# Kernel optimization log

Hardware: AMD Instinct MI355X
Metric: run time of the kernel (lower is better)

## Reference

```python
import jax, jax.numpy as jnp
import numpy as np

B, S = 2, 1024
V, D, H, L, F, M = 50257, 768, 12, 6, 3072, 1024
DK = D // H
EPS = 1e-5


def _layer_norm(x, g, b):
    mu = jnp.mean(x, axis=-1, keepdims=True)
    var = jnp.mean(jnp.square(x - mu), axis=-1, keepdims=True)
    return (x - mu) * jax.lax.rsqrt(var + EPS) * g + b


def setup_inputs() -> dict:
    key = jax.random.key(0)
    ks = jax.random.split(key, 20)
    std = 0.02
    inp = {
        'input_ids': jax.random.randint(ks[0], (B, S), 0, V),
        'tok_emb': jax.random.normal(ks[1], (V, D), jnp.float32) * std,
        'pos_emb': jax.random.normal(ks[2], (M, D), jnp.float32) * std,
        # per-layer stacked params; linear weights stored as [in, out] (y = x @ W)
        'wq': jax.random.normal(ks[3], (L, D, D), jnp.float32) * std,
        'wk': jax.random.normal(ks[4], (L, D, D), jnp.float32) * std,
        'wv': jax.random.normal(ks[5], (L, D, D), jnp.float32) * std,
        'wo': jax.random.normal(ks[6], (L, D, D), jnp.float32) * std,
        'bo': jnp.zeros((L, D), jnp.float32),
        'fc_w': jax.random.normal(ks[7], (L, D, F), jnp.float32) * std,
        'fc_b': jnp.zeros((L, F), jnp.float32),
        'proj_w': jax.random.normal(ks[8], (L, F, D), jnp.float32) * std,
        'proj_b': jnp.zeros((L, D), jnp.float32),
        'ln1_g': jnp.ones((L, D), jnp.float32),
        'ln1_b': jnp.zeros((L, D), jnp.float32),
        'ln2_g': jnp.ones((L, D), jnp.float32),
        'ln2_b': jnp.zeros((L, D), jnp.float32),
        'lnf_g': jnp.ones((D,), jnp.float32),
        'lnf_b': jnp.zeros((D,), jnp.float32),
        'out_w': jax.random.normal(ks[9], (D, V), jnp.float32) * std,
    }
    return inp


def reference(input_ids, tok_emb, pos_emb, wq, wk, wv, wo, bo, fc_w, fc_b,
              proj_w, proj_b, ln1_g, ln1_b, ln2_g, ln2_b, lnf_g, lnf_b, out_w):
    b, s = input_ids.shape
    x = tok_emb[input_ids] + pos_emb[jnp.arange(s)][None, :, :]  # [B,S,D]
    causal = jnp.tril(jnp.ones((s, s), bool))  # [S,S]
    scale = 1.0 / np.sqrt(DK)
    for l in range(L):
        xn = _layer_norm(x, ln1_g[l], ln1_b[l])
        q = (xn @ wq[l]).reshape(b, s, H, DK).transpose(0, 2, 1, 3)
        k = (xn @ wk[l]).reshape(b, s, H, DK).transpose(0, 2, 1, 3)
        v = (xn @ wv[l]).reshape(b, s, H, DK).transpose(0, 2, 1, 3)
        scores = jnp.einsum('bhqd,bhkd->bhqk', q, k) * scale
        scores = jnp.where(causal[None, None], scores, -1e9)
        attn = jax.nn.softmax(scores, axis=-1)
        ctx = jnp.einsum('bhqk,bhkd->bhqd', attn, v)
        ctx = ctx.transpose(0, 2, 1, 3).reshape(b, s, D)
        x = x + ctx @ wo[l] + bo[l]
        xn = _layer_norm(x, ln2_g[l], ln2_b[l])
        h = jax.nn.gelu(xn @ fc_w[l] + fc_b[l], approximate=False)
        x = x + h @ proj_w[l] + proj_b[l]
    x = _layer_norm(x, lnf_g, lnf_b)
    logits = x @ out_w  # [B,S,V]
    return logits
```

## Files before the change

kernel.cpp:

```cpp
#include <hip/hip_runtime.h>
#include <hip/hip_bf16.h>
#include <math.h>

#define BB 2
#define SS 1024
#define DD 768
#define HH 12
#define LL 6
#define FF 3072
#define VV 50257
#define DKK 64
#define NROWS (BB * SS)
#define QKVN (3 * DD)
#define QBLK 64
#define KVBLK 64

#define OFF_QKV 0
#define OFF_WO  1769472
#define OFF_FC  2359296
#define OFF_PROJ 4718592
#define PL      7077888

typedef __attribute__((ext_vector_type(8))) short short8v;
typedef __attribute__((ext_vector_type(4))) float f32x4;
typedef __attribute__((ext_vector_type(4))) int int4v;

__device__ __forceinline__ float gelu_f(float x) {
    return 0.5f * x * (1.0f + erff(x * 0.70710678118654752440f));
}

__device__ __forceinline__ void gload16(const void* g, void* l) {
    __builtin_amdgcn_global_load_lds(
        (const __attribute__((address_space(1))) void*)g,
        (__attribute__((address_space(3))) void*)l, 16, 0, 0);
}

__global__ __launch_bounds__(256) void embed_kernel(
    const int* __restrict__ ids, const float* __restrict__ tok,
    const float* __restrict__ pos, float* __restrict__ x) {
    int row = blockIdx.x;
    int s = row & (SS - 1);
    int id = ids[row];
    const float* t = tok + (size_t)id * DD;
    const float* p = pos + (size_t)s * DD;
    float* xr = x + (size_t)row * DD;
    for (int i = threadIdx.x; i < DD; i += 256)
        xr[i] = t[i] + p[i];
}

__global__ __launch_bounds__(256) void ln_kernel(
    const float* __restrict__ x, const float* __restrict__ g,
    const float* __restrict__ b, float* __restrict__ out) {
    int row = blockIdx.x;
    int tid = threadIdx.x;
    const float* xr = x + (size_t)row * DD;
    float v0 = xr[tid], v1 = xr[tid + 256], v2 = xr[tid + 512];
    __shared__ float red[256];
    red[tid] = v0 + v1 + v2;
    __syncthreads();
    for (int s2 = 128; s2 > 0; s2 >>= 1) {
        if (tid < s2) red[tid] += red[tid + s2];
        __syncthreads();
    }
    float mu = red[0] * (1.0f / DD);
    __syncthreads();
    float d0 = v0 - mu, d1 = v1 - mu, d2 = v2 - mu;
    red[tid] = d0 * d0 + d1 * d1 + d2 * d2;
    __syncthreads();
    for (int s2 = 128; s2 > 0; s2 >>= 1) {
        if (tid < s2) red[tid] += red[tid + s2];
        __syncthreads();
    }
    float r = rsqrtf(red[0] * (1.0f / DD) + 1e-5f);
    float* o = out + (size_t)row * DD;
    o[tid]       = d0 * r * g[tid]       + b[tid];
    o[tid + 256] = d1 * r * g[tid + 256] + b[tid + 256];
    o[tid + 512] = d2 * r * g[tid + 512] + b[tid + 512];
}

__global__ __launch_bounds__(256) void ln_bf16_kernel(
    const float* __restrict__ x, const float* __restrict__ g,
    const float* __restrict__ b, __hip_bfloat16* __restrict__ out) {
    int row = blockIdx.x;
    int tid = threadIdx.x;
    const float* xr = x + (size_t)row * DD;
    float v0 = xr[tid], v1 = xr[tid + 256], v2 = xr[tid + 512];
    __shared__ float red[256];
    red[tid] = v0 + v1 + v2;
    __syncthreads();
    for (int s2 = 128; s2 > 0; s2 >>= 1) {
        if (tid < s2) red[tid] += red[tid + s2];
        __syncthreads();
    }
    float mu = red[0] * (1.0f / DD);
    __syncthreads();
    float d0 = v0 - mu, d1 = v1 - mu, d2 = v2 - mu;
    red[tid] = d0 * d0 + d1 * d1 + d2 * d2;
    __syncthreads();
    for (int s2 = 128; s2 > 0; s2 >>= 1) {
        if (tid < s2) red[tid] += red[tid + s2];
        __syncthreads();
    }
    float r = rsqrtf(red[0] * (1.0f / DD) + 1e-5f);
    __hip_bfloat16* o = out + (size_t)row * DD;
    o[tid]       = __float2bfloat16(d0 * r * g[tid]       + b[tid]);
    o[tid + 256] = __float2bfloat16(d1 * r * g[tid + 256] + b[tid + 256]);
    o[tid + 512] = __float2bfloat16(d2 * r * g[tid + 512] + b[tid + 512]);
}

__global__ __launch_bounds__(256) void transpose_cvt_kernel(
    const float* __restrict__ W, __hip_bfloat16* __restrict__ Wt, int K, int N) {
    __shared__ float t[32][33];
    int bn = blockIdx.x * 32, bk = blockIdx.y * 32;
    int tx = threadIdx.x & 31, ty = threadIdx.x >> 5;
    for (int r = ty; r < 32; r += 8)
        t[r][tx] = (bn + tx < N) ? W[(size_t)(bk + r) * N + bn + tx] : 0.0f;
    __syncthreads();
    for (int r = ty; r < 32; r += 8) {
        int n = bn + r;
        if (n < N) Wt[(size_t)n * K + bk + tx] = __float2bfloat16(t[tx][r]);
    }
}

__global__ __launch_bounds__(256) void transpose_all_kernel(
    const float* __restrict__ wq, const float* __restrict__ wk,
    const float* __restrict__ wv, const float* __restrict__ wo,
    const float* __restrict__ fc_w, const float* __restrict__ proj_w,
    const float* __restrict__ out_w, __hip_bfloat16* __restrict__ Wt_all) {
    int bid = blockIdx.x;
    const float* W;
    __hip_bfloat16* Wt;
    int K, N, tn, tk;
    if (bid < 6 * 6912) {
        int l = bid / 6912, r = bid % 6912;
        __hip_bfloat16* base = Wt_all + (size_t)l * PL;
        if (r < 1728) {
            int which = r / 576, idx = r % 576;
            W = (which == 0 ? wq : (which == 1 ? wk : wv)) + (size_t)l * DD * DD;
            Wt = base + (size_t)which * DD * DD;
            K = DD; N = DD; tn = idx % 24; tk = idx / 24;
        } else if (r < 2304) {
            int idx = r - 1728;
            W = wo + (size_t)l * DD * DD;
            Wt = base + OFF_WO;
            K = DD; N = DD; tn = idx % 24; tk = idx / 24;
        } else if (r < 4608) {
            int idx = r - 2304;
            W = fc_w + (size_t)l * DD * FF;
            Wt = base + OFF_FC;
            K = DD; N = FF; tn = idx % 96; tk = idx / 96;
        } else {
            int idx = r - 4608;
            W = proj_w + (size_t)l * FF * DD;
            Wt = base + OFF_PROJ;
            K = FF; N = DD; tn = idx % 24; tk = idx / 24;
        }
    } else {
        int idx = bid - 6 * 6912;
        W = out_w;
        Wt = Wt_all + (size_t)6 * PL;
        K = DD; N = VV; tn = idx % 1571; tk = idx / 1571;
    }
    __shared__ float t[32][33];
    int bn = tn * 32, bk = tk * 32;
    int tx = threadIdx.x & 31, ty = threadIdx.x >> 5;
    for (int r = ty; r < 32; r += 8)
        t[r][tx] = (bn + tx < N) ? W[(size_t)(bk + r) * N + bn + tx] : 0.0f;
    __syncthreads();
    for (int r = ty; r < 32; r += 8) {
        int n = bn + r;
        if (n < N) Wt[(size_t)n * K + bk + tx] = __float2bfloat16(t[tx][r]);
    }
}

#define SWZ128(row, byteoff) \
    ((row) * 128 + (((((byteoff) >> 4) ^ ((row) & 7)) & 7) << 4) + ((byteoff) & 15))

__device__ __forceinline__ void tile_remap(int mtiles, int BM, int BN, int& bm, int& bn) {
    const int nblk = gridDim.x;
    int hw = blockIdx.x, j = hw;
    if ((nblk & 7) == 0) j = (hw & 7) * (nblk >> 3) + (hw >> 3);
    bm = (j % mtiles) * BM;
    bn = (j / mtiles) * BN;
}

template<int BM, int BN>
__global__ __launch_bounds__(256) void gemm_mfma_kernel(
    const __hip_bfloat16* __restrict__ A, const __hip_bfloat16* __restrict__ Wt,
    const float* __restrict__ bias, const float* __restrict__ residual,
    float* __restrict__ Cf, __hip_bfloat16* __restrict__ Cb,
    int M, int N, int K, int do_gelu, int mtiles) {
    constexpr int BK = 32;
    constexpr int UA = (BM * 4) / 256;
    constexpr int UB = (BN * 4) / 256;
    constexpr int FM = BM / 32;
    constexpr int FN = BN / 32;
    __shared__ __align__(16) char As[BM * 64];
    __shared__ __align__(16) char Bs[BN * 64];

    const int tid = threadIdx.x;
    const int lane = tid & 63;
    const int wid = tid >> 6;
    int bm, bn;
    tile_remap(mtiles, BM, BN, bm, bn);
    const int r16 = lane & 15;
    const int kg = lane >> 4;
    const int wm = (wid >> 1) * (FM * 16);
    const int wn = (wid & 1) * (FN * 16);

    f32x4 acc[FM][FN];
    const f32x4 zf = {0.0f, 0.0f, 0.0f, 0.0f};
#pragma unroll
    for (int i = 0; i < FM; ++i)
#pragma unroll
        for (int j = 0; j < FN; ++j) acc[i][j] = zf;

    for (int k0 = 0; k0 < K; k0 += BK) {
        __syncthreads();
#pragma unroll
        for (int u = 0; u < UA; ++u) {
            int cb = wid * 64 + u * 256;
            int c = cb + lane;
            gload16(A + (size_t)(bm + (c >> 2)) * K + k0 + (c & 3) * 8,
                    As + cb * 16);
        }
#pragma unroll
        for (int u = 0; u < UB; ++u) {
            int cb = wid * 64 + u * 256;
            int c = cb + lane;
            gload16(Wt + (size_t)(bn + (c >> 2)) * K + k0 + (c & 3) * 8,
                    Bs + cb * 16);
        }
        __syncthreads();

        short8v af[FM], bfr[FN];
#pragma unroll
        for (int i = 0; i < FM; ++i)
            af[i] = *(const short8v*)(As + (wm + i * 16 + r16) * 64 + kg * 16);
#pragma unroll
        for (int j = 0; j < FN; ++j)
            bfr[j] = *(const short8v*)(Bs + (wn + j * 16 + r16) * 64 + kg * 16);
#pragma unroll
        for (int i = 0; i < FM; ++i)
#pragma unroll
            for (int j = 0; j < FN; ++j)
                acc[i][j] = __builtin_amdgcn_mfma_f32_16x16x32_bf16(
                    af[i], bfr[j], acc[i][j], 0, 0, 0);
    }

    const int rg = lane >> 4;
#pragma unroll
    for (int i = 0; i < FM; ++i) {
#pragma unroll
        for (int j = 0; j < FN; ++j) {
            int col = bn + wn + j * 16 + r16;
            if (col < N) {
#pragma unroll
                for (int r = 0; r < 4; ++r) {
                    int row = bm + wm + i * 16 + rg * 4 + r;
                    float v = acc[i][j][r];
                    if (bias) v += bias[col];
                    if (do_gelu) v = gelu_f(v);
                    size_t o = (size_t)row * N + col;
                    if (residual) v += residual[o];
                    if (Cf) Cf[o] = v;
                    else Cb[o] = __float2bfloat16(v);
                }
            }
        }
    }
}

__global__ __launch_bounds__(256) void qkv_gemm_kernel(
    const __hip_bfloat16* __restrict__ A, const __hip_bfloat16* __restrict__ Wt,
    __hip_bfloat16* __restrict__ qh, __hip_bfloat16* __restrict__ kh,
    __hip_bfloat16* __restrict__ vt) {
    constexpr int BM = 128, BN = 128, BK = 32;
    constexpr int K = DD;
    constexpr int FM = 4, FN = 4;
    __shared__ __align__(16) char As[BM * 64];
    __shared__ __align__(16) char Bs[BN * 64];

    const int tid = threadIdx.x;
    const int lane = tid & 63;
    const int wid = tid >> 6;
    int bm, bn;
    tile_remap(16, BM, BN, bm, bn);
    const int r16 = lane & 15;
    const int kg = lane >> 4;
    const int wm = (wid >> 1) * 64;
    const int wn = (wid & 1) * 64;

    f32x4 acc[FM][FN];
    const f32x4 zf = {0.0f, 0.0f, 0.0f, 0.0f};
#pragma unroll
    for (int i = 0; i < FM; ++i)
#pragma unroll
        for (int j = 0; j < FN; ++j) acc[i][j] = zf;

    for (int k0 = 0; k0 < K; k0 += BK) {
        __syncthreads();
#pragma unroll
        for (int u = 0; u < 2; ++u) {
            int cb = wid * 64 + u * 256;
            int c = cb + lane;
            gload16(A + (size_t)(bm + (c >> 2)) * K + k0 + (c & 3) * 8,
                    As + cb * 16);
        }
#pragma unroll
        for (int u = 0; u < 2; ++u) {
            int cb = wid * 64 + u * 256;
            int c = cb + lane;
            gload16(Wt + (size_t)(bn + (c >> 2)) * K + k0 + (c & 3) * 8,
                    Bs + cb * 16);
        }
        __syncthreads();

        short8v af[FM], bfr[FN];
#pragma unroll
        for (int i = 0; i < FM; ++i)
            af[i] = *(const short8v*)(As + (wm + i * 16 + r16) * 64 + kg * 16);
#pragma unroll
        for (int j = 0; j < FN; ++j)
            bfr[j] = *(const short8v*)(Bs + (wn + j * 16 + r16) * 64 + kg * 16);
#pragma unroll
        for (int i = 0; i < FM; ++i)
#pragma unroll
            for (int j = 0; j < FN; ++j)
                acc[i][j] = __builtin_amdgcn_mfma_f32_16x16x32_bf16(
                    af[i], bfr[j], acc[i][j], 0, 0, 0);
    }

#pragma unroll
    for (int i = 0; i < FM; ++i) {
#pragma unroll
        for (int j = 0; j < FN; ++j) {
            int col = bn + wn + j * 16 + r16;
#pragma unroll
            for (int r = 0; r < 4; ++r) {
                int row = bm + wm + i * 16 + kg * 4 + r;
                int b = row >> 10, s = row & (SS - 1);
                float v = acc[i][j][r];
                if (col < DD) {
                    int h = col >> 6, d = col & 63;
                    qh[((size_t)(b * HH + h) * SS + s) * DKK + d] =
                        __float2bfloat16(v * 0.125f);
                } else if (col < 2 * DD) {
                    int c = col - DD, h = c >> 6, d = c & 63;
                    kh[((size_t)(b * HH + h) * SS + s) * DKK + d] = __float2bfloat16(v);
                } else {
                    int c = col - 2 * DD, h = c >> 6, d = c & 63;
                    vt[((size_t)(b * HH + h) * DKK + d) * SS + s] = __float2bfloat16(v);
                }
            }
        }
    }
}

__global__ __launch_bounds__(256) void flash_attn_kernel(
    const __hip_bfloat16* __restrict__ qh, const __hip_bfloat16* __restrict__ kh,
    const __hip_bfloat16* __restrict__ vt, __hip_bfloat16* __restrict__ ctx) {
    __shared__ __align__(16) char Ks[KVBLK * 128];
    __shared__ __align__(16) char Vs[DKK * 128];
    __shared__ __align__(16) char Ps[4][16 * 128];

    const int bh = blockIdx.x;
    const int qt = (gridDim.y - 1) - blockIdx.y;
    const int q0 = qt * QBLK;
    const int b = bh / HH;
    const int h = bh - b * HH;
    const int tid = threadIdx.x;
    const int lane = tid & 63;
    const int w = tid >> 6;
    const int r16 = lane & 15;
    const int kg = lane >> 4;
    char* Pw = Ps[w];

    const size_t qbase = ((size_t)bh * SS + q0 + w * 16 + r16) * DKK;
    short8v qf0 = *(const short8v*)(qh + qbase + kg * 8);
    short8v qf1 = *(const short8v*)(qh + qbase + 32 + kg * 8);

    f32x4 acc_o[4];
    const f32x4 zf = {0.0f, 0.0f, 0.0f, 0.0f};
    float m[4], l[4];
#pragma unroll
    for (int j = 0; j < 4; ++j) acc_o[j] = zf;
#pragma unroll
    for (int r = 0; r < 4; ++r) { m[r] = -1e30f; l[r] = 0.0f; }

    const int nt = qt + 1;
    for (int t = 0; t < nt; ++t) {
        __syncthreads();
        {
            const __hip_bfloat16* kp = kh + ((size_t)bh * SS + t * KVBLK) * DKK;
            const __hip_bfloat16* vp = vt + (size_t)bh * DKK * SS + t * KVBLK;
#pragma unroll
            for (int u = 0; u < 2; ++u) {
                int c = tid + u * 256;
                int row = c >> 3, slot = c & 7;
                *(int4v*)(Ks + SWZ128(row, slot * 16)) =
                    *(const int4v*)(kp + (size_t)row * DKK + slot * 8);
                *(int4v*)(Vs + SWZ128(row, slot * 16)) =
                    *(const int4v*)(vp + (size_t)row * SS + slot * 8);
            }
        }
        __syncthreads();

        f32x4 s[4];
#pragma unroll
        for (int j = 0; j < 4; ++j) s[j] = zf;
#pragma unroll
        for (int j = 0; j < 4; ++j) {
            short8v k0f = *(const short8v*)(Ks + SWZ128(j * 16 + r16, kg * 16));
            short8v k1f = *(const short8v*)(Ks + SWZ128(j * 16 + r16, 64 + kg * 16));
            s[j] = __builtin_amdgcn_mfma_f32_16x16x32_bf16(qf0, k0f, s[j], 0, 0, 0);
            s[j] = __builtin_amdgcn_mfma_f32_16x16x32_bf16(qf1, k1f, s[j], 0, 0, 0);
        }

        if (t == qt) {
#pragma unroll
            for (int j = 0; j < 4; ++j)
#pragma unroll
                for (int r = 0; r < 4; ++r)
                    if (j * 16 + r16 > w * 16 + kg * 4 + r) s[j][r] = -1e30f;
        }

        float alpha[4], rsum[4];
#pragma unroll
        for (int r = 0; r < 4; ++r) {
            float v = fmaxf(fmaxf(s[0][r], s[1][r]), fmaxf(s[2][r], s[3][r]));
#pragma unroll
            for (int d2 = 1; d2 < 16; d2 <<= 1)
                v = fmaxf(v, __shfl_xor(v, d2));
            float mnew = fmaxf(m[r], v);
            alpha[r] = __expf(m[r] - mnew);
            m[r] = mnew;
            rsum[r] = 0.0f;
        }
#pragma unroll
        for (int j = 0; j < 4; ++j)
#pragma unroll
            for (int r = 0; r < 4; ++r) {
                float p = __expf(s[j][r] - m[r]);
                rsum[r] += p;
                *(__hip_bfloat16*)(Pw + SWZ128(kg * 4 + r, (j * 16 + r16) * 2)) =
                    __float2bfloat16(p);
            }
#pragma unroll
        for (int r = 0; r < 4; ++r) {
#pragma unroll
            for (int d2 = 1; d2 < 16; d2 <<= 1)
                rsum[r] += __shfl_xor(rsum[r], d2);
            l[r] = l[r] * alpha[r] + rsum[r];
        }
#pragma unroll
        for (int j = 0; j < 4; ++j)
#pragma unroll
            for (int r = 0; r < 4; ++r) acc_o[j][r] *= alpha[r];

        short8v pa0 = *(const short8v*)(Pw + SWZ128(r16, kg * 16));
        short8v pa1 = *(const short8v*)(Pw + SWZ128(r16, 64 + kg * 16));
#pragma unroll
        for (int j = 0; j < 4; ++j) {
            short8v v0f = *(const short8v*)(Vs + SWZ128(j * 16 + r16, kg * 16));
            short8v v1f = *(const short8v*)(Vs + SWZ128(j * 16 + r16, 64 + kg * 16));
            acc_o[j] = __builtin_amdgcn_mfma_f32_16x16x32_bf16(pa0, v0f, acc_o[j], 0, 0, 0);
            acc_o[j] = __builtin_amdgcn_mfma_f32_16x16x32_bf16(pa1, v1f, acc_o[j], 0, 0, 0);
        }
    }

#pragma unroll
    for (int r = 0; r < 4; ++r) {
        float inv = 1.0f / l[r];
        int row = q0 + w * 16 + kg * 4 + r;
        __hip_bfloat16* cp = ctx + ((size_t)(b * SS) + row) * DD + h * DKK;
#pragma unroll
        for (int j = 0; j < 4; ++j)
            cp[j * 16 + r16] = __float2bfloat16(acc_o[j][r] * inv);
    }
}

__global__ __launch_bounds__(256) void gemm_kernel(
    const float* __restrict__ A, const float* __restrict__ W,
    const float* __restrict__ bias, const float* __restrict__ residual,
    float* __restrict__ C, int M, int N, int K, int do_gelu) {
    __shared__ float As[16][64];
    __shared__ float Ws[16][68];
    int tid = threadIdx.x;
    int bn = blockIdx.x * 64, bm = blockIdx.y * 64;
    int tx = tid & 15, ty = tid >> 4;
    int ar = tid >> 2, ak = (tid & 3) << 2;
    int wr = tid >> 4, wc = (tid & 15) << 2;
    bool n_vec = ((N & 3) == 0);
    float acc[4][4] = {};
    for (int k0 = 0; k0 < K; k0 += 16) {
        float4 av = *(const float4*)&A[(size_t)(bm + ar) * K + (k0 + ak)];
        As[ak + 0][ar] = av.x; As[ak + 1][ar] = av.y;
        As[ak + 2][ar] = av.z; As[ak + 3][ar] = av.w;
        int gn = bn + wc;
        const float* wp = &W[(size_t)(k0 + wr) * N + gn];
        float w0, w1, w2, w3;
        if (n_vec && gn + 3 < N) {
            float4 wv4 = *(const float4*)wp;
            w0 = wv4.x; w1 = wv4.y; w2 = wv4.z; w3 = wv4.w;
        } else {
            w0 = (gn + 0 < N) ? wp[0] : 0.0f;
            w1 = (gn + 1 < N) ? wp[1] : 0.0f;
            w2 = (gn + 2 < N) ? wp[2] : 0.0f;
            w3 = (gn + 3 < N) ? wp[3] : 0.0f;
        }
        Ws[wr][wc + 0] = w0; Ws[wr][wc + 1] = w1;
        Ws[wr][wc + 2] = w2; Ws[wr][wc + 3] = w3;
        __syncthreads();
#pragma unroll
        for (int kk = 0; kk < 16; ++kk) {
            float a[4], w[4];
#pragma unroll
            for (int i = 0; i < 4; ++i) a[i] = As[kk][ty * 4 + i];
#pragma unroll
            for (int j = 0; j < 4; ++j) w[j] = Ws[kk][tx * 4 + j];
#pragma unroll
            for (int i = 0; i < 4; ++i)
#pragma unroll
                for (int j = 0; j < 4; ++j)
                    acc[i][j] = fmaf(a[i], w[j], acc[i][j]);
        }
        __syncthreads();
    }
#pragma unroll
    for (int i = 0; i < 4; ++i) {
        int row = bm + ty * 4 + i;
#pragma unroll
        for (int j = 0; j < 4; ++j) {
            int col = bn + tx * 4 + j;
            if (col < N) {
                float val = acc[i][j];
                if (bias) val += bias[col];
                if (do_gelu) val = gelu_f(val);
                if (residual) val += residual[(size_t)row * N + col];
                C[(size_t)row * N + col] = val;
            }
        }
    }
}

__global__ __launch_bounds__(256) void attn_kernel(
    const float* __restrict__ q, const float* __restrict__ k,
    const float* __restrict__ v, float* __restrict__ ctx) {
    int bid = blockIdx.x;
    int qi = bid & (SS - 1);
    int bh = bid >> 10;
    int h = bh % HH;
    int b = bh / HH;
    int tid = threadIdx.x;
    __shared__ float qs[DKK];
    __shared__ float p[SS];
    __shared__ float red[256];
    __shared__ float ctx_red[4][DKK];
    const float* qrow = q + ((size_t)(b * SS + qi)) * DD + h * DKK;
    if (tid < DKK) qs[tid] = qrow[tid];
    __syncthreads();
    int nk = qi + 1;
    const float scale = 0.125f;
    for (int ki = tid; ki < nk; ki += 256) {
        const float* krow = k + ((size_t)(b * SS + ki)) * DD + h * DKK;
        float dot = 0.0f;
#pragma unroll
        for (int d = 0; d < DKK; d += 4) {
            float4 kv = *(const float4*)&krow[d];
            dot += qs[d] * kv.x + qs[d + 1] * kv.y + qs[d + 2] * kv.z + qs[d + 3] * kv.w;
        }
        p[ki] = dot * scale;
    }
    __syncthreads();
    float lmax = -1e30f;
    for (int ki = tid; ki < nk; ki += 256) lmax = fmaxf(lmax, p[ki]);
    red[tid] = lmax;
    __syncthreads();
    for (int s2 = 128; s2 > 0; s2 >>= 1) {
        if (tid < s2) red[tid] = fmaxf(red[tid], red[tid + s2]);
        __syncthreads();
    }
    float mm = red[0];
    __syncthreads();
    float lsum = 0.0f;
    for (int ki = tid; ki < nk; ki += 256) {
        float e = __expf(p[ki] - mm);
        p[ki] = e;
        lsum += e;
    }
    red[tid] = lsum;
    __syncthreads();
    for (int s2 = 128; s2 > 0; s2 >>= 1) {
        if (tid < s2) red[tid] += red[tid + s2];
        __syncthreads();
    }
    float inv = 1.0f / red[0];
    int d = tid & 63;
    int chunk = tid >> 6;
    float accd = 0.0f;
    for (int ki = chunk; ki < nk; ki += 4)
        accd += p[ki] * v[((size_t)(b * SS + ki)) * DD + h * DKK + d];
    ctx_red[chunk][d] = accd;
    __syncthreads();
    if (tid < DKK) {
        float sum = (ctx_red[0][tid] + ctx_red[1][tid]) + (ctx_red[2][tid] + ctx_red[3][tid]);
        ctx[((size_t)(b * SS + qi)) * DD + h * DKK + tid] = sum * inv;
    }
}

extern "C" void kernel_launch(void* const* d_in, const int* in_sizes, int n_in,
                              void* d_out, int out_size, void* d_ws, size_t ws_size,
                              hipStream_t stream) {
    const int*   ids    = (const int*)  d_in[0];
    const float* tok    = (const float*)d_in[1];
    const float* pos    = (const float*)d_in[2];
    const float* wq     = (const float*)d_in[3];
    const float* wk     = (const float*)d_in[4];
    const float* wv     = (const float*)d_in[5];
    const float* wo     = (const float*)d_in[6];
    const float* bo     = (const float*)d_in[7];
    const float* fc_w   = (const float*)d_in[8];
    const float* fc_b   = (const float*)d_in[9];
    const float* proj_w = (const float*)d_in[10];
    const float* proj_b = (const float*)d_in[11];
    const float* ln1_g  = (const float*)d_in[12];
    const float* ln1_b  = (const float*)d_in[13];
    const float* ln2_g  = (const float*)d_in[14];
    const float* ln2_b  = (const float*)d_in[15];
    const float* lnf_g  = (const float*)d_in[16];
    const float* lnf_b  = (const float*)d_in[17];
    const float* out_w  = (const float*)d_in[18];
    float* out = (float*)d_out;

    dim3 blk(256);

    const size_t SZ_X    = (size_t)NROWS * DD * 4;
    const size_t SZ_XN   = (size_t)NROWS * DD * 2;
    const size_t SZ_HD   = (size_t)BB * HH * SS * DKK * 2;
    const size_t SZ_CTX  = (size_t)NROWS * DD * 2;
    const size_t SZ_H    = (size_t)NROWS * FF * 2;
    const size_t SZ_WT1  = (size_t)50304 * DD * 2;
    const size_t SZ_WTA  = ((size_t)6 * PL + (size_t)50304 * DD) * 2;
    const size_t ACT     = SZ_X + SZ_XN + 3 * SZ_HD + SZ_CTX + SZ_H;
    const size_t NEED_MID = ACT + SZ_WT1;
    const size_t NEED_BIG = ACT + SZ_WTA;

    if (ws_size >= NEED_MID) {
        const bool big = (ws_size >= NEED_BIG);
        char* p = (char*)d_ws;
        float*          x    = (float*)p;          p += SZ_X;
        __hip_bfloat16* xn   = (__hip_bfloat16*)p; p += SZ_XN;
        __hip_bfloat16* qhb  = (__hip_bfloat16*)p; p += SZ_HD;
        __hip_bfloat16* khb  = (__hip_bfloat16*)p; p += SZ_HD;
        __hip_bfloat16* vtb  = (__hip_bfloat16*)p; p += SZ_HD;
        __hip_bfloat16* ctx  = (__hip_bfloat16*)p; p += SZ_CTX;
        __hip_bfloat16* hbuf = (__hip_bfloat16*)p; p += SZ_H;
        __hip_bfloat16* Wt   = (__hip_bfloat16*)p;

        dim3 tD(DD / 32, DD / 32);
        dim3 tF(FF / 32, DD / 32);
        dim3 tP(DD / 32, FF / 32);
        dim3 tV((VV + 31) / 32, DD / 32);

        const int nQKV = (QKVN / 128) * (NROWS / 128);
        const int nFC  = (FF / 128) * (NROWS / 128);
        const int nWO  = (DD / 64) * (NROWS / 64);
        const int nV   = ((VV + 127) / 128) * (NROWS / 128);
        dim3 gA(BB * HH, SS / QBLK);

        if (big)
            transpose_all_kernel<<<6 * 6912 + 37704, blk, 0, stream>>>(
                wq, wk, wv, wo, fc_w, proj_w, out_w, Wt);

        embed_kernel<<<NROWS, blk, 0, stream>>>(ids, tok, pos, x);

        for (int l = 0; l < LL; ++l) {
            __hip_bfloat16* qkvWt = big ? Wt + (size_t)l * PL : Wt;
            __hip_bfloat16* woWt  = big ? Wt + (size_t)l * PL + OFF_WO : Wt;
            __hip_bfloat16* fcWt  = big ? Wt + (size_t)l * PL + OFF_FC : Wt;
            __hip_bfloat16* pjWt  = big ? Wt + (size_t)l * PL + OFF_PROJ : Wt;

            ln_bf16_kernel<<<NROWS, blk, 0, stream>>>(x, ln1_g + l * DD, ln1_b + l * DD, xn);
            if (!big) {
                transpose_cvt_kernel<<<tD, blk, 0, stream>>>(wq + (size_t)l * DD * DD, qkvWt, DD, DD);
                transpose_cvt_kernel<<<tD, blk, 0, stream>>>(wk + (size_t)l * DD * DD, qkvWt + (size_t)DD * DD, DD, DD);
                transpose_cvt_kernel<<<tD, blk, 0, stream>>>(wv + (size_t)l * DD * DD, qkvWt + (size_t)2 * DD * DD, DD, DD);
            }
            qkv_gemm_kernel<<<nQKV, blk, 0, stream>>>(xn, qkvWt, qhb, khb, vtb);
            flash_attn_kernel<<<gA, blk, 0, stream>>>(qhb, khb, vtb, ctx);
            if (!big)
                transpose_cvt_kernel<<<tD, blk, 0, stream>>>(wo + (size_t)l * DD * DD, woWt, DD, DD);
            gemm_mfma_kernel<64, 64><<<nWO, blk, 0, stream>>>(
                ctx, woWt, bo + l * DD, x, x, nullptr, NROWS, DD, DD, 0, NROWS / 64);
            ln_bf16_kernel<<<NROWS, blk, 0, stream>>>(x, ln2_g + l * DD, ln2_b + l * DD, xn);
            if (!big)
                transpose_cvt_kernel<<<tF, blk, 0, stream>>>(fc_w + (size_t)l * DD * FF, fcWt, DD, FF);
            gemm_mfma_kernel<128, 128><<<nFC, blk, 0, stream>>>(
                xn, fcWt, fc_b + l * FF, nullptr, nullptr, hbuf, NROWS, FF, DD, 1, NROWS / 128);
            if (!big)
                transpose_cvt_kernel<<<tP, blk, 0, stream>>>(proj_w + (size_t)l * FF * DD, pjWt, FF, DD);
            gemm_mfma_kernel<64, 64><<<nWO, blk, 0, stream>>>(
                hbuf, pjWt, proj_b + l * DD, x, x, nullptr, NROWS, DD, FF, 0, NROWS / 64);
        }

        __hip_bfloat16* outWt = big ? Wt + (size_t)6 * PL : Wt;
        ln_bf16_kernel<<<NROWS, blk, 0, stream>>>(x, lnf_g, lnf_b, xn);
        if (!big)
            transpose_cvt_kernel<<<tV, blk, 0, stream>>>(out_w, outWt, DD, VV);
        gemm_mfma_kernel<128, 128><<<nV, blk, 0, stream>>>(
            xn, outWt, nullptr, nullptr, out, nullptr, NROWS, VV, DD, 0, NROWS / 128);
        return;
    }

    const size_t XSZ = (size_t)NROWS * DD;
    float* ws = (float*)d_ws;
    float* x  = ws;
    float* xn = x  + XSZ;
    float* qb = xn + XSZ;
    float* kb = qb + XSZ;
    float* vb = kb + XSZ;
    float* cb = vb + XSZ;
    float* hb = cb + XSZ;

    dim3 gD((DD + 63) / 64, NROWS / 64);
    dim3 gF((FF + 63) / 64, NROWS / 64);
    dim3 gV2((VV + 63) / 64, NROWS / 64);

    embed_kernel<<<NROWS, blk, 0, stream>>>(ids, tok, pos, x);
    for (int l = 0; l < LL; ++l) {
        const float* wq_l = wq + (size_t)l * DD * DD;
        const float* wk_l = wk + (size_t)l * DD * DD;
        const float* wv_l = wv + (size_t)l * DD * DD;
        const float* wo_l = wo + (size_t)l * DD * DD;
        const float* fc_w_l = fc_w + (size_t)l * DD * FF;
        const float* pj_w_l = proj_w + (size_t)l * FF * DD;
        ln_kernel<<<NROWS, blk, 0, stream>>>(x, ln1_g + l * DD, ln1_b + l * DD, xn);
        gemm_kernel<<<gD, blk, 0, stream>>>(xn, wq_l, nullptr, nullptr, qb, NROWS, DD, DD, 0);
        gemm_kernel<<<gD, blk, 0, stream>>>(xn, wk_l, nullptr, nullptr, kb, NROWS, DD, DD, 0);
        gemm_kernel<<<gD, blk, 0, stream>>>(xn, wv_l, nullptr, nullptr, vb, NROWS, DD, DD, 0);
        attn_kernel<<<BB * HH * SS, blk, 0, stream>>>(qb, kb, vb, cb);
        gemm_kernel<<<gD, blk, 0, stream>>>(cb, wo_l, bo + l * DD, x, x, NROWS, DD, DD, 0);
        ln_kernel<<<NROWS, blk, 0, stream>>>(x, ln2_g + l * DD, ln2_b + l * DD, xn);
        gemm_kernel<<<gF, blk, 0, stream>>>(xn, fc_w_l, fc_b + l * FF, nullptr, hb, NROWS, FF, DD, 1);
        gemm_kernel<<<gD, blk, 0, stream>>>(hb, pj_w_l, proj_b + l * DD, x, x, NROWS, DD, FF, 0);
    }
    ln_kernel<<<NROWS, blk, 0, stream>>>(x, lnf_g, lnf_b, xn);
    gemm_kernel<<<gV2, blk, 0, stream>>>(xn, out_w, nullptr, nullptr, out, NROWS, VV, DD, 0);
}
```

Measured before the change: 1.681 ms.

## Software-pipeline GEMM loads through registers with double-buffered swizzled LDS

Replaces the direct global-to-LDS loads with register prefetch two k-steps ahead, written into two alternating LDS buffers with an XOR swizzle. This drops one barrier per k-step and overlaps global memory latency with MFMA work. The swizzle is meant to cut LDS bank conflicts on fragment reads. In exchange it uses more registers and twice the LDS, which may lower occupancy, and it assumes K/32 is even.

New measurement: 1.599 ms. -4.9%, faster.

```diff
diff --git a/kernel.cpp b/kernel.cpp
--- a/kernel.cpp
+++ b/kernel.cpp
@@ -27,12 +27,6 @@
 
 __device__ __forceinline__ float gelu_f(float x) {
     return 0.5f * x * (1.0f + erff(x * 0.70710678118654752440f));
-}
-
-__device__ __forceinline__ void gload16(const void* g, void* l) {
-    __builtin_amdgcn_global_load_lds(
-        (const __attribute__((address_space(1))) void*)g,
-        (__attribute__((address_space(3))) void*)l, 16, 0, 0);
 }
 
 __global__ __launch_bounds__(256) void embed_kernel(
@@ -173,6 +167,7 @@
     }
 }
 
+#define LDSOFF(row, ks) (((row) * 64) + ((((ks) ^ (((row) >> 1) & 3))) << 4))
 #define SWZ128(row, byteoff) \
     ((row) * 128 + (((((byteoff) >> 4) ^ ((row) & 7)) & 7) << 4) + ((byteoff) & 15))
 
@@ -184,19 +179,57 @@
     bn = (j / mtiles) * BN;
 }
 
+#define GSTEP(ASB, BSB, AR, BR, IT)                                            \
+    {                                                                          \
+        _Pragma("unroll") for (int u = 0; u < UA; ++u) {                       \
+            int c = tid + u * 256, row = c >> 2, sl = c & 3;                   \
+            *(int4v*)(ASB + LDSOFF(row, sl)) = AR[u];                          \
+        }                                                                      \
+        _Pragma("unroll") for (int u = 0; u < UB; ++u) {                       \
+            int c = tid + u * 256, row = c >> 2, sl = c & 3;                   \
+            *(int4v*)(BSB + LDSOFF(row, sl)) = BR[u];                          \
+        }                                                                      \
+        __syncthreads();                                                       \
+        {                                                                      \
+            int kn = ((IT) + 2) * 32;                                          \
+            if (kn < K) {                                                      \
+                _Pragma("unroll") for (int u = 0; u < UA; ++u) {               \
+                    int c = tid + u * 256, row = c >> 2, sl = c & 3;           \
+                    AR[u] = *(const int4v*)(A + (size_t)(bm + row) * K + kn + sl * 8); \
+                }                                                              \
+                _Pragma("unroll") for (int u = 0; u < UB; ++u) {               \
+                    int c = tid + u * 256, row = c >> 2, sl = c & 3;           \
+                    int4v bv = zi;                                             \
+                    if (bn + row < N) bv = *(const int4v*)(Wt + (size_t)(bn + row) * K + kn + sl * 8); \
+                    BR[u] = bv;                                                \
+                }                                                              \
+            }                                                                  \
+        }                                                                      \
+        short8v af[FM], bfr[FN];                                               \
+        _Pragma("unroll") for (int i = 0; i < FM; ++i)                         \
+            af[i] = *(const short8v*)(ASB + LDSOFF(wm + i * 16 + r16, kg));    \
+        _Pragma("unroll") for (int j = 0; j < FN; ++j)                         \
+            bfr[j] = *(const short8v*)(BSB + LDSOFF(wn + j * 16 + r16, kg));   \
+        _Pragma("unroll") for (int i = 0; i < FM; ++i)                         \
+            _Pragma("unroll") for (int j = 0; j < FN; ++j)                     \
+                acc[i][j] = __builtin_amdgcn_mfma_f32_16x16x32_bf16(           \
+                    af[i], bfr[j], acc[i][j], 0, 0, 0);                        \
+    }
+
 template<int BM, int BN>
 __global__ __launch_bounds__(256) void gemm_mfma_kernel(
     const __hip_bfloat16* __restrict__ A, const __hip_bfloat16* __restrict__ Wt,
     const float* __restrict__ bias, const float* __restrict__ residual,
     float* __restrict__ Cf, __hip_bfloat16* __restrict__ Cb,
     int M, int N, int K, int do_gelu, int mtiles) {
-    constexpr int BK = 32;
     constexpr int UA = (BM * 4) / 256;
     constexpr int UB = (BN * 4) / 256;
     constexpr int FM = BM / 32;
     constexpr int FN = BN / 32;
-    __shared__ __align__(16) char As[BM * 64];
-    __shared__ __align__(16) char Bs[BN * 64];
+    __shared__ __align__(16) char As0[BM * 64];
+    __shared__ __align__(16) char Bs0[BN * 64];
+    __shared__ __align__(16) char As1[BM * 64];
+    __shared__ __align__(16) char Bs1[BN * 64];
 
     const int tid = threadIdx.x;
     const int lane = tid & 63;
@@ -215,37 +248,30 @@
 #pragma unroll
         for (int j = 0; j < FN; ++j) acc[i][j] = zf;
 
-    for (int k0 = 0; k0 < K; k0 += BK) {
-        __syncthreads();
-#pragma unroll
-        for (int u = 0; u < UA; ++u) {
-            int cb = wid * 64 + u * 256;
-            int c = cb + lane;
-            gload16(A + (size_t)(bm + (c >> 2)) * K + k0 + (c & 3) * 8,
-                    As + cb * 16);
-        }
-#pragma unroll
-        for (int u = 0; u < UB; ++u) {
-            int cb = wid * 64 + u * 256;
-            int c = cb + lane;
-            gload16(Wt + (size_t)(bn + (c >> 2)) * K + k0 + (c & 3) * 8,
-                    Bs + cb * 16);
-        }
-        __syncthreads();
-
-        short8v af[FM], bfr[FN];
-#pragma unroll
-        for (int i = 0; i < FM; ++i)
-            af[i] = *(const short8v*)(As + (wm + i * 16 + r16) * 64 + kg * 16);
-#pragma unroll
-        for (int j = 0; j < FN; ++j)
-            bfr[j] = *(const short8v*)(Bs + (wn + j * 16 + r16) * 64 + kg * 16);
-#pragma unroll
-        for (int i = 0; i < FM; ++i)
-#pragma unroll
-            for (int j = 0; j < FN; ++j)
-                acc[i][j] = __builtin_amdgcn_mfma_f32_16x16x32_bf16(
-                    af[i], bfr[j], acc[i][j], 0, 0, 0);
+    int4v areg0[UA], areg1[UA], breg0[UB], breg1[UB];
+    const int4v zi = {0, 0, 0, 0};
+
+#pragma unroll
+    for (int u = 0; u < UA; ++u) {
+        int c = tid + u * 256, row = c >> 2, sl = c & 3;
+        areg0[u] = *(const int4v*)(A + (size_t)(bm + row) * K + sl * 8);
+        areg1[u] = *(const int4v*)(A + (size_t)(bm + row) * K + 32 + sl * 8);
+    }
+#pragma unroll
+    for (int u = 0; u < UB; ++u) {
+        int c = tid + u * 256, row = c >> 2, sl = c & 3;
+        int4v b0 = zi, b1 = zi;
+        if (bn + row < N) {
+            b0 = *(const int4v*)(Wt + (size_t)(bn + row) * K + sl * 8);
+            b1 = *(const int4v*)(Wt + (size_t)(bn + row) * K + 32 + sl * 8);
+        }
+        breg0[u] = b0; breg1[u] = b1;
+    }
+
+    const int NIT = K >> 5;
+    for (int it = 0; it < NIT; it += 2) {
+        GSTEP(As0, Bs0, areg0, breg0, it);
+        GSTEP(As1, Bs1, areg1, breg1, it + 1);
     }
 
     const int rg = lane >> 4;
@@ -275,11 +301,13 @@
     const __hip_bfloat16* __restrict__ A, const __hip_bfloat16* __restrict__ Wt,
     __hip_bfloat16* __restrict__ qh, __hip_bfloat16* __restrict__ kh,
     __hip_bfloat16* __restrict__ vt) {
-    constexpr int BM = 128, BN = 128, BK = 32;
-    constexpr int K = DD;
-    constexpr int FM = 4, FN = 4;
-    __shared__ __align__(16) char As[BM * 64];
-    __shared__ __align__(16) char Bs[BN * 64];
+    constexpr int BM = 128, BN = 128;
+    constexpr int K = DD, N = QKVN;
+    constexpr int UA = 2, UB = 2, FM = 4, FN = 4;
+    __shared__ __align__(16) char As0[BM * 64];
+    __shared__ __align__(16) char Bs0[BN * 64];
+    __shared__ __align__(16) char As1[BM * 64];
+    __shared__ __align__(16) char Bs1[BN * 64];
 
     const int tid = threadIdx.x;
     const int lane = tid & 63;
@@ -298,37 +326,22 @@
 #pragma unroll
         for (int j = 0; j < FN; ++j) acc[i][j] = zf;
 
-    for (int k0 = 0; k0 < K; k0 += BK) {
-        __syncthreads();
-#pragma unroll
-        for (int u = 0; u < 2; ++u) {
-            int cb = wid * 64 + u * 256;
-            int c = cb + lane;
-            gload16(A + (size_t)(bm + (c >> 2)) * K + k0 + (c & 3) * 8,
-                    As + cb * 16);
-        }
-#pragma unroll
-        for (int u = 0; u < 2; ++u) {
-            int cb = wid * 64 + u * 256;
-            int c = cb + lane;
-            gload16(Wt + (size_t)(bn + (c >> 2)) * K + k0 + (c & 3) * 8,
-                    Bs + cb * 16);
-        }
-        __syncthreads();
-
-        short8v af[FM], bfr[FN];
-#pragma unroll
-        for (int i = 0; i < FM; ++i)
-            af[i] = *(const short8v*)(As + (wm + i * 16 + r16) * 64 + kg * 16);
-#pragma unroll
-        for (int j = 0; j < FN; ++j)
-            bfr[j] = *(const short8v*)(Bs + (wn + j * 16 + r16) * 64 + kg * 16);
-#pragma unroll
-        for (int i = 0; i < FM; ++i)
-#pragma unroll
-            for (int j = 0; j < FN; ++j)
-                acc[i][j] = __builtin_amdgcn_mfma_f32_16x16x32_bf16(
-                    af[i], bfr[j], acc[i][j], 0, 0, 0);
+    int4v areg0[UA], areg1[UA], breg0[UB], breg1[UB];
+    const int4v zi = {0, 0, 0, 0};
+
+#pragma unroll
+    for (int u = 0; u < UA; ++u) {
+        int c = tid + u * 256, row = c >> 2, sl = c & 3;
+        areg0[u] = *(const int4v*)(A + (size_t)(bm + row) * K + sl * 8);
+        areg1[u] = *(const int4v*)(A + (size_t)(bm + row) * K + 32 + sl * 8);
+        breg0[u] = *(const int4v*)(Wt + (size_t)(bn + row) * K + sl * 8);
+        breg1[u] = *(const int4v*)(Wt + (size_t)(bn + row) * K + 32 + sl * 8);
+    }
+
+    const int NIT = K >> 5;
+    for (int it = 0; it < NIT; it += 2) {
+        GSTEP(As0, Bs0, areg0, breg0, it);
+        GSTEP(As1, Bs1, areg1, breg1, it + 1);
     }
 
 #pragma unroll
```
